# Kernel optimization log

Hardware: AMD Instinct MI355X
Metric: run time of the kernel (lower is better)

The kernel has to match this reference:

```python
import jax, jax.numpy as jnp
import numpy as np
from math import sqrt

B, S, E, D, O = 8, 2048, 1024, 128, 1024


def setup_inputs() -> dict:
    key = jax.random.key(0)
    ks = jax.random.split(key, 12)
    inp = {
        "query": jax.random.normal(ks[0], (B, S, E), jnp.float32),
        "key": jax.random.normal(ks[1], (B, S, E), jnp.float32),
        "value": jax.random.normal(ks[2], (B, S, E), jnp.float32),
        # causal (lower-triangular) mask, broadcastable over batch
        "mask": jnp.tril(jnp.ones((S, S), jnp.int32))[None, :, :],
        # linear params (torch Linear: y = x @ W.T + b); store as [in, out]
        "Wq": jax.random.normal(ks[3], (E, D), jnp.float32) / sqrt(E),
        "bq": jnp.zeros((D,), jnp.float32),
        "Wk": jax.random.normal(ks[4], (E, D), jnp.float32) / sqrt(E),
        "bk": jnp.zeros((D,), jnp.float32),
        "Wv": jax.random.normal(ks[5], (E, D), jnp.float32) / sqrt(E),
        "bv": jnp.zeros((D,), jnp.float32),
        "Wo": jax.random.normal(ks[6], (D, O), jnp.float32) / sqrt(D),
        "bo": jnp.zeros((O,), jnp.float32),
    }
    return inp


def reference(query, key, value, mask, Wq, bq, Wk, bk, Wv, bv, Wo, bo):
    q = jnp.einsum("bse,ed->bsd", query, Wq) + bq
    k = jnp.einsum("bse,ed->bsd", key, Wk) + bk
    v = jnp.einsum("bse,ed->bsd", value, Wv) + bv
    scale = 1.0 / sqrt(q.shape[-1])
    scores = jnp.einsum("bqd,bkd->bqk", q, k) * scale  # [B,S,S]
    scores = jnp.where(mask == 0, -jnp.inf, scores)
    weights = jax.nn.softmax(scores, axis=-1)
    weights = jnp.nan_to_num(weights)  # fully-masked rows -> 0, matching torch
    out = jnp.einsum("bqk,bkd->bqd", weights, v)
    return jnp.einsum("bqd,do->bqo", out, Wo) + bo
```

## Files before the change

kernel.cpp:

```cpp
#include <hip/hip_runtime.h>
#include <hip/hip_bf16.h>
#include <math.h>

#define B_ 8
#define S_ 2048
#define E_ 1024
#define D_ 128
#define O_ 1024
#define M_ (B_*S_)

typedef __bf16 bf16x8 __attribute__((ext_vector_type(8)));
typedef __bf16 bf16x4 __attribute__((ext_vector_type(4)));
typedef float  f32x4  __attribute__((ext_vector_type(4)));

#define MFMA16(a,b,c) __builtin_amdgcn_mfma_f32_16x16x32_bf16((a),(b),(c),0,0,0)

__global__ __launch_bounds__(256) void k_prep_weights(
    const float* __restrict__ Wq, const float* __restrict__ Wk,
    const float* __restrict__ Wv, const float* __restrict__ Wo,
    __bf16* __restrict__ Wtq, __bf16* __restrict__ Wtk,
    __bf16* __restrict__ Wtv, __bf16* __restrict__ Wot)
{
    const int bid = blockIdx.x;
    const int job = bid >> 7;
    const int within = bid & 127;

    const float* in;
    __bf16* outp;
    int R, C, bx, by;
    if (job < 3) {
        R = E_; C = D_;
        bx = within & 3; by = within >> 2;
        in   = (job == 0) ? Wq  : (job == 1) ? Wk  : Wv;
        outp = (job == 0) ? Wtq : (job == 1) ? Wtk : Wtv;
    } else {
        R = D_; C = O_;
        bx = within & 31; by = within >> 5;
        in = Wo; outp = Wot;
    }

    __shared__ float tile[32][33];
    const int tx = threadIdx.x, ty = threadIdx.y;
    int x = bx * 32 + tx;
    #pragma unroll
    for (int i = 0; i < 4; ++i) {
        int y = by * 32 + ty + i * 8;
        tile[ty + i * 8][tx] = in[(size_t)y * C + x];
    }
    __syncthreads();
    int xo = by * 32 + tx;
    #pragma unroll
    for (int i = 0; i < 4; ++i) {
        int yo = bx * 32 + ty + i * 8;
        outp[(size_t)yo * R + xo] = (__bf16)tile[tx][ty + i * 8];
    }
}

__global__ __launch_bounds__(256) void k_qkv_proj(
    const float* __restrict__ Xq, const float* __restrict__ Xk, const float* __restrict__ Xv,
    const __bf16* __restrict__ Wtq, const __bf16* __restrict__ Wtk, const __bf16* __restrict__ Wtv,
    const float* __restrict__ bq, const float* __restrict__ bk, const float* __restrict__ bv,
    __bf16* __restrict__ Qb, __bf16* __restrict__ Kb, __bf16* __restrict__ Vt)
{
    const int z = blockIdx.y;
    const float*  X    = (z == 0) ? Xq  : (z == 1) ? Xk  : Xv;
    const __bf16* Wt   = (z == 0) ? Wtq : (z == 1) ? Wtk : Wtv;
    const float*  bias = (z == 0) ? bq  : (z == 1) ? bk  : bv;

    __shared__ __align__(16) __bf16 As[128][40];
    __shared__ __align__(16) __bf16 Bs[128][40];

    const int tid  = threadIdx.x;
    const int lane = tid & 63;
    const int w    = tid >> 6;
    const int wr   = w >> 1, wc = w & 1;
    const int g    = lane >> 4, lr = lane & 15;
    const int m0   = blockIdx.x * 128;

    f32x4 acc[4][4] = {};

    for (int k0 = 0; k0 < E_; k0 += 32) {
        #pragma unroll
        for (int i = 0; i < 4; ++i) {
            int f = tid + i * 256;
            int row = f >> 3, c4 = f & 7;
            float4 v = *reinterpret_cast<const float4*>(X + (size_t)(m0 + row) * E_ + k0 + c4 * 4);
            bf16x4 h = { (__bf16)v.x, (__bf16)v.y, (__bf16)v.z, (__bf16)v.w };
            *reinterpret_cast<bf16x4*>(&As[row][c4 * 4]) = h;
        }
        #pragma unroll
        for (int i = 0; i < 2; ++i) {
            int f = tid + i * 256;
            int row = f >> 2, c8 = f & 3;
            bf16x8 v = *reinterpret_cast<const bf16x8*>(Wt + (size_t)row * E_ + k0 + c8 * 8);
            *reinterpret_cast<bf16x8*>(&Bs[row][c8 * 8]) = v;
        }
        __syncthreads();
        bf16x8 af[4], bfr[4];
        #pragma unroll
        for (int mi = 0; mi < 4; ++mi)
            af[mi] = *reinterpret_cast<const bf16x8*>(&As[wr * 64 + mi * 16 + lr][g * 8]);
        #pragma unroll
        for (int ni = 0; ni < 4; ++ni)
            bfr[ni] = *reinterpret_cast<const bf16x8*>(&Bs[wc * 64 + ni * 16 + lr][g * 8]);
        #pragma unroll
        for (int mi = 0; mi < 4; ++mi)
            #pragma unroll
            for (int ni = 0; ni < 4; ++ni)
                acc[mi][ni] = MFMA16(af[mi], bfr[ni], acc[mi][ni]);
        __syncthreads();
    }

    #pragma unroll
    for (int mi = 0; mi < 4; ++mi) {
        #pragma unroll
        for (int ni = 0; ni < 4; ++ni) {
            #pragma unroll
            for (int r = 0; r < 4; ++r) {
                int row = m0 + wr * 64 + mi * 16 + 4 * g + r;
                int col = wc * 64 + ni * 16 + lr;
                float v = acc[mi][ni][r] + bias[col];
                if (z == 0)      Qb[(size_t)row * D_ + col] = (__bf16)v;
                else if (z == 1) Kb[(size_t)row * D_ + col] = (__bf16)v;
                else {
                    int b = row >> 11, s = row & (S_ - 1);
                    Vt[((size_t)b * D_ + col) * S_ + s] = (__bf16)v;
                }
            }
        }
    }
}

__global__ __launch_bounds__(256) void k_attn(
    const __bf16* __restrict__ Q, const __bf16* __restrict__ K,
    const __bf16* __restrict__ Vt, __bf16* __restrict__ Ab)
{
    __shared__ __align__(16) __bf16 Ks[2][64][136];
    __shared__ __align__(16) __bf16 Vs[2][128][72];
    __shared__ __align__(16) __bf16 P[4][16][72];

    const int tid  = threadIdx.x;
    const int lane = tid & 63;
    const int w    = tid >> 6;
    const int g    = lane >> 4, lr = lane & 15;

    const int b     = blockIdx.x & 7;
    const int tq    = blockIdx.x >> 3;
    const int qbase = tq * 64;
    const int nch   = tq + 1;

    const __bf16* Qp  = Q  + (size_t)b * S_ * D_;
    const __bf16* Kp  = K  + (size_t)b * S_ * D_;
    const __bf16* Vtp = Vt + (size_t)b * D_ * S_;

    const float NEG_INF = -__builtin_inff();
    const float scale   = 0.08838834764831845f;

    const int krow = tid >> 2, kcb = (tid & 3) * 32;
    const int vrow = tid >> 1, vcb = (tid & 1) * 32;

    bf16x8 qf[4];
    #pragma unroll
    for (int dc = 0; dc < 4; ++dc)
        qf[dc] = *reinterpret_cast<const bf16x8*>(
            Qp + (size_t)(qbase + w * 16 + lr) * D_ + dc * 32 + g * 8);

    f32x4 o[8] = {};
    float m[4], l[4];
    #pragma unroll
    for (int r = 0; r < 4; ++r) { m[r] = NEG_INF; l[r] = 0.f; }

    bf16x8 kreg[4], vreg[4];

    {
        const __bf16* ks = Kp + (size_t)krow * D_ + kcb;
        const __bf16* vs = Vtp + (size_t)vrow * S_ + vcb;
        #pragma unroll
        for (int i = 0; i < 4; ++i) kreg[i] = *reinterpret_cast<const bf16x8*>(ks + i * 8);
        #pragma unroll
        for (int i = 0; i < 4; ++i) vreg[i] = *reinterpret_cast<const bf16x8*>(vs + i * 8);
        #pragma unroll
        for (int i = 0; i < 4; ++i) *reinterpret_cast<bf16x8*>(&Ks[0][krow][kcb + i * 8]) = kreg[i];
        #pragma unroll
        for (int i = 0; i < 4; ++i) *reinterpret_cast<bf16x8*>(&Vs[0][vrow][vcb + i * 8]) = vreg[i];
    }
    __syncthreads();

    for (int j = 0; j < nch; ++j) {
        const int  buf = j & 1;
        const bool pre = (j + 1 < nch);

        if (pre) {
            const int kv1 = (j + 1) * 64;
            const __bf16* ks = Kp + (size_t)(kv1 + krow) * D_ + kcb;
            const __bf16* vs = Vtp + (size_t)vrow * S_ + kv1 + vcb;
            #pragma unroll
            for (int i = 0; i < 4; ++i) kreg[i] = *reinterpret_cast<const bf16x8*>(ks + i * 8);
            #pragma unroll
            for (int i = 0; i < 4; ++i) vreg[i] = *reinterpret_cast<const bf16x8*>(vs + i * 8);
        }

        f32x4 s[4] = {};
        #pragma unroll
        for (int c = 0; c < 4; ++c) {
            #pragma unroll
            for (int dc = 0; dc < 4; ++dc) {
                bf16x8 kf = *reinterpret_cast<const bf16x8*>(&Ks[buf][c * 16 + lr][dc * 32 + g * 8]);
                s[c] = MFMA16(qf[dc], kf, s[c]);
            }
        }

        float p[4][4];
        float mt[4] = { NEG_INF, NEG_INF, NEG_INF, NEG_INF };
        if (j == tq) {
            #pragma unroll
            for (int c = 0; c < 4; ++c)
                #pragma unroll
                for (int r = 0; r < 4; ++r) {
                    float v = (c * 16 + lr <= w * 16 + 4 * g + r) ? s[c][r] * scale : NEG_INF;
                    p[c][r] = v;
                    mt[r] = fmaxf(mt[r], v);
                }
        } else {
            #pragma unroll
            for (int c = 0; c < 4; ++c)
                #pragma unroll
                for (int r = 0; r < 4; ++r) {
                    float v = s[c][r] * scale;
                    p[c][r] = v;
                    mt[r] = fmaxf(mt[r], v);
                }
        }
        #pragma unroll
        for (int off = 1; off < 16; off <<= 1)
            #pragma unroll
            for (int r = 0; r < 4; ++r)
                mt[r] = fmaxf(mt[r], __shfl_xor(mt[r], off));

        float corr[4], ts[4] = {0.f, 0.f, 0.f, 0.f};
        #pragma unroll
        for (int r = 0; r < 4; ++r) {
            float mn = fmaxf(m[r], mt[r]);
            corr[r] = __expf(m[r] - mn);
            m[r] = mn;
        }
        #pragma unroll
        for (int c = 0; c < 4; ++c)
            #pragma unroll
            for (int r = 0; r < 4; ++r) {
                float e = __expf(p[c][r] - m[r]);
                p[c][r] = e;
                ts[r] += e;
            }
        #pragma unroll
        for (int off = 1; off < 16; off <<= 1)
            #pragma unroll
            for (int r = 0; r < 4; ++r)
                ts[r] += __shfl_xor(ts[r], off);
        #pragma unroll
        for (int r = 0; r < 4; ++r) l[r] = l[r] * corr[r] + ts[r];
        #pragma unroll
        for (int dt = 0; dt < 8; ++dt)
            #pragma unroll
            for (int r = 0; r < 4; ++r)
                o[dt][r] *= corr[r];

        #pragma unroll
        for (int c = 0; c < 4; ++c)
            #pragma unroll
            for (int r = 0; r < 4; ++r)
                P[w][4 * g + r][c * 16 + lr] = (__bf16)p[c][r];
        bf16x8 pf[2];
        #pragma unroll
        for (int kc = 0; kc < 2; ++kc)
            pf[kc] = *reinterpret_cast<const bf16x8*>(&P[w][lr][kc * 32 + g * 8]);

        #pragma unroll
        for (int dt = 0; dt < 8; ++dt) {
            #pragma unroll
            for (int kc = 0; kc < 2; ++kc) {
                bf16x8 vf = *reinterpret_cast<const bf16x8*>(&Vs[buf][dt * 16 + lr][kc * 32 + g * 8]);
                o[dt] = MFMA16(pf[kc], vf, o[dt]);
            }
        }

        if (pre) {
            const int nb = buf ^ 1;
            #pragma unroll
            for (int i = 0; i < 4; ++i) *reinterpret_cast<bf16x8*>(&Ks[nb][krow][kcb + i * 8]) = kreg[i];
            #pragma unroll
            for (int i = 0; i < 4; ++i) *reinterpret_cast<bf16x8*>(&Vs[nb][vrow][vcb + i * 8]) = vreg[i];
            __syncthreads();
        }
    }

    float inv[4];
    #pragma unroll
    for (int r = 0; r < 4; ++r) inv[r] = 1.f / l[r];
    #pragma unroll
    for (int dt = 0; dt < 8; ++dt)
        #pragma unroll
        for (int r = 0; r < 4; ++r)
            Ab[((size_t)b * S_ + qbase + w * 16 + 4 * g + r) * D_ + dt * 16 + lr] =
                (__bf16)(o[dt][r] * inv[r]);
}

__global__ __launch_bounds__(256) void k_out_proj(
    const __bf16* __restrict__ A, const __bf16* __restrict__ Wot,
    const float* __restrict__ bo, float* __restrict__ out)
{
    __shared__ __align__(16) __bf16 As[128][40];
    __shared__ __align__(16) __bf16 Bs[128][40];

    const int tid  = threadIdx.x;
    const int lane = tid & 63;
    const int w    = tid >> 6;
    const int wr   = w >> 1, wc = w & 1;
    const int g    = lane >> 4, lr = lane & 15;
    const int m0   = blockIdx.x * 128;
    const int n0   = blockIdx.y * 128;

    f32x4 acc[4][4] = {};

    #pragma unroll
    for (int k0 = 0; k0 < D_; k0 += 32) {
        #pragma unroll
        for (int i = 0; i < 2; ++i) {
            int f = tid + i * 256;
            int row = f >> 2, c8 = f & 3;
            *reinterpret_cast<bf16x8*>(&As[row][c8 * 8]) =
                *reinterpret_cast<const bf16x8*>(A + (size_t)(m0 + row) * D_ + k0 + c8 * 8);
            *reinterpret_cast<bf16x8*>(&Bs[row][c8 * 8]) =
                *reinterpret_cast<const bf16x8*>(Wot + (size_t)(n0 + row) * D_ + k0 + c8 * 8);
        }
        __syncthreads();
        bf16x8 af[4], bfr[4];
        #pragma unroll
        for (int mi = 0; mi < 4; ++mi)
            af[mi] = *reinterpret_cast<const bf16x8*>(&As[wr * 64 + mi * 16 + lr][g * 8]);
        #pragma unroll
        for (int ni = 0; ni < 4; ++ni)
            bfr[ni] = *reinterpret_cast<const bf16x8*>(&Bs[wc * 64 + ni * 16 + lr][g * 8]);
        #pragma unroll
        for (int mi = 0; mi < 4; ++mi)
            #pragma unroll
            for (int ni = 0; ni < 4; ++ni)
                acc[mi][ni] = MFMA16(af[mi], bfr[ni], acc[mi][ni]);
        __syncthreads();
    }

    #pragma unroll
    for (int mi = 0; mi < 4; ++mi)
        #pragma unroll
        for (int ni = 0; ni < 4; ++ni)
            #pragma unroll
            for (int r = 0; r < 4; ++r) {
                int row = m0 + wr * 64 + mi * 16 + 4 * g + r;
                int col = n0 + wc * 64 + ni * 16 + lr;
                out[(size_t)row * O_ + col] = acc[mi][ni][r] + bo[col];
            }
}

extern "C" void kernel_launch(void* const* d_in, const int* in_sizes, int n_in,
                              void* d_out, int out_size, void* d_ws, size_t ws_size,
                              hipStream_t stream)
{
    const float* query = (const float*)d_in[0];
    const float* key   = (const float*)d_in[1];
    const float* value = (const float*)d_in[2];
    const float* Wq = (const float*)d_in[4];
    const float* bq = (const float*)d_in[5];
    const float* Wk = (const float*)d_in[6];
    const float* bk = (const float*)d_in[7];
    const float* Wv = (const float*)d_in[8];
    const float* bv = (const float*)d_in[9];
    const float* Wo = (const float*)d_in[10];
    const float* bo = (const float*)d_in[11];
    float* out = (float*)d_out;

    __bf16* Qb  = (__bf16*)d_ws;
    __bf16* Kb  = Qb  + (size_t)M_ * D_;
    __bf16* Vt  = Kb  + (size_t)M_ * D_;
    __bf16* Ab  = Vt  + (size_t)M_ * D_;
    __bf16* Wtq = Ab  + (size_t)M_ * D_;
    __bf16* Wtk = Wtq + (size_t)E_ * D_;
    __bf16* Wtv = Wtk + (size_t)E_ * D_;
    __bf16* Wot = Wtv + (size_t)E_ * D_;

    k_prep_weights<<<512, dim3(32, 8), 0, stream>>>(Wq, Wk, Wv, Wo, Wtq, Wtk, Wtv, Wot);

    k_qkv_proj<<<dim3(M_ / 128, 3), 256, 0, stream>>>(
        query, key, value, Wtq, Wtk, Wtv, bq, bk, bv, Qb, Kb, Vt);

    k_attn<<<256, 256, 0, stream>>>(Qb, Kb, Vt, Ab);

    k_out_proj<<<dim3(M_ / 128, O_ / 128), 256, 0, stream>>>(Ab, Wot, bo, out);
}
```

Measured before the change: 335.8 us.

## Double-buffer QKV projection with register prefetch and halve M tile

The QKV projection kernel now prefetches the next K-slice of activations and weights into registers while MFMAs run on the current shared-memory buffer, then writes into a second LDS buffer with one barrier per iteration. The M tile shrinks from 128 to 64 rows, doubling the grid to raise occupancy and wave count across CUs. The aim is to hide global-load latency on this memory-bound fp32-input GEMM, at the cost of more weight re-reads per block and extra register use.

```diff
diff --git a/kernel.cpp b/kernel.cpp
--- a/kernel.cpp
+++ b/kernel.cpp
@@ -67,57 +67,83 @@
     const __bf16* Wt   = (z == 0) ? Wtq : (z == 1) ? Wtk : Wtv;
     const float*  bias = (z == 0) ? bq  : (z == 1) ? bk  : bv;
 
-    __shared__ __align__(16) __bf16 As[128][40];
-    __shared__ __align__(16) __bf16 Bs[128][40];
+    __shared__ __align__(16) __bf16 As[2][64][40];
+    __shared__ __align__(16) __bf16 Bs[2][128][40];
 
     const int tid  = threadIdx.x;
     const int lane = tid & 63;
     const int w    = tid >> 6;
     const int wr   = w >> 1, wc = w & 1;
     const int g    = lane >> 4, lr = lane & 15;
-    const int m0   = blockIdx.x * 128;
-
-    f32x4 acc[4][4] = {};
-
-    for (int k0 = 0; k0 < E_; k0 += 32) {
-        #pragma unroll
-        for (int i = 0; i < 4; ++i) {
-            int f = tid + i * 256;
-            int row = f >> 3, c4 = f & 7;
-            float4 v = *reinterpret_cast<const float4*>(X + (size_t)(m0 + row) * E_ + k0 + c4 * 4);
-            bf16x4 h = { (__bf16)v.x, (__bf16)v.y, (__bf16)v.z, (__bf16)v.w };
-            *reinterpret_cast<bf16x4*>(&As[row][c4 * 4]) = h;
-        }
-        #pragma unroll
-        for (int i = 0; i < 2; ++i) {
-            int f = tid + i * 256;
-            int row = f >> 2, c8 = f & 3;
-            bf16x8 v = *reinterpret_cast<const bf16x8*>(Wt + (size_t)row * E_ + k0 + c8 * 8);
-            *reinterpret_cast<bf16x8*>(&Bs[row][c8 * 8]) = v;
-        }
-        __syncthreads();
-        bf16x8 af[4], bfr[4];
-        #pragma unroll
-        for (int mi = 0; mi < 4; ++mi)
-            af[mi] = *reinterpret_cast<const bf16x8*>(&As[wr * 64 + mi * 16 + lr][g * 8]);
+    const int m0   = blockIdx.x * 64;
+
+    const int ar0 = tid >> 3,          ac0 = (tid & 7) * 4;
+    const int ar1 = (tid + 256) >> 3,  ac1 = ac0;
+    const int br0 = tid >> 2,          bc0 = (tid & 3) * 8;
+    const int br1 = (tid + 256) >> 2,  bc1 = bc0;
+
+    f32x4 acc[2][4] = {};
+    float4 areg0, areg1;
+    bf16x8 breg0, breg1;
+
+    areg0 = *reinterpret_cast<const float4*>(X + (size_t)(m0 + ar0) * E_ + ac0);
+    areg1 = *reinterpret_cast<const float4*>(X + (size_t)(m0 + ar1) * E_ + ac1);
+    breg0 = *reinterpret_cast<const bf16x8*>(Wt + (size_t)br0 * E_ + bc0);
+    breg1 = *reinterpret_cast<const bf16x8*>(Wt + (size_t)br1 * E_ + bc1);
+    {
+        bf16x4 h0 = { (__bf16)areg0.x, (__bf16)areg0.y, (__bf16)areg0.z, (__bf16)areg0.w };
+        bf16x4 h1 = { (__bf16)areg1.x, (__bf16)areg1.y, (__bf16)areg1.z, (__bf16)areg1.w };
+        *reinterpret_cast<bf16x4*>(&As[0][ar0][ac0]) = h0;
+        *reinterpret_cast<bf16x4*>(&As[0][ar1][ac1]) = h1;
+        *reinterpret_cast<bf16x8*>(&Bs[0][br0][bc0]) = breg0;
+        *reinterpret_cast<bf16x8*>(&Bs[0][br1][bc1]) = breg1;
+    }
+    __syncthreads();
+
+    for (int j = 0; j < E_ / 32; ++j) {
+        const int  buf = j & 1;
+        const bool pre = (j + 1 < E_ / 32);
+
+        if (pre) {
+            const int k1 = (j + 1) * 32;
+            areg0 = *reinterpret_cast<const float4*>(X + (size_t)(m0 + ar0) * E_ + k1 + ac0);
+            areg1 = *reinterpret_cast<const float4*>(X + (size_t)(m0 + ar1) * E_ + k1 + ac1);
+            breg0 = *reinterpret_cast<const bf16x8*>(Wt + (size_t)br0 * E_ + k1 + bc0);
+            breg1 = *reinterpret_cast<const bf16x8*>(Wt + (size_t)br1 * E_ + k1 + bc1);
+        }
+
+        bf16x8 af[2], bfr[4];
+        #pragma unroll
+        for (int mi = 0; mi < 2; ++mi)
+            af[mi] = *reinterpret_cast<const bf16x8*>(&As[buf][wr * 32 + mi * 16 + lr][g * 8]);
         #pragma unroll
         for (int ni = 0; ni < 4; ++ni)
-            bfr[ni] = *reinterpret_cast<const bf16x8*>(&Bs[wc * 64 + ni * 16 + lr][g * 8]);
-        #pragma unroll
-        for (int mi = 0; mi < 4; ++mi)
+            bfr[ni] = *reinterpret_cast<const bf16x8*>(&Bs[buf][wc * 64 + ni * 16 + lr][g * 8]);
+        #pragma unroll
+        for (int mi = 0; mi < 2; ++mi)
             #pragma unroll
             for (int ni = 0; ni < 4; ++ni)
                 acc[mi][ni] = MFMA16(af[mi], bfr[ni], acc[mi][ni]);
-        __syncthreads();
-    }
-
-    #pragma unroll
-    for (int mi = 0; mi < 4; ++mi) {
+
+        if (pre) {
+            const int nb = buf ^ 1;
+            bf16x4 h0 = { (__bf16)areg0.x, (__bf16)areg0.y, (__bf16)areg0.z, (__bf16)areg0.w };
+            bf16x4 h1 = { (__bf16)areg1.x, (__bf16)areg1.y, (__bf16)areg1.z, (__bf16)areg1.w };
+            *reinterpret_cast<bf16x4*>(&As[nb][ar0][ac0]) = h0;
+            *reinterpret_cast<bf16x4*>(&As[nb][ar1][ac1]) = h1;
+            *reinterpret_cast<bf16x8*>(&Bs[nb][br0][bc0]) = breg0;
+            *reinterpret_cast<bf16x8*>(&Bs[nb][br1][bc1]) = breg1;
+            __syncthreads();
+        }
+    }
+
+    #pragma unroll
+    for (int mi = 0; mi < 2; ++mi) {
         #pragma unroll
         for (int ni = 0; ni < 4; ++ni) {
             #pragma unroll
             for (int r = 0; r < 4; ++r) {
-                int row = m0 + wr * 64 + mi * 16 + 4 * g + r;
+                int row = m0 + wr * 32 + mi * 16 + 4 * g + r;
                 int col = wc * 64 + ni * 16 + lr;
                 float v = acc[mi][ni][r] + bias[col];
                 if (z == 0)      Qb[(size_t)row * D_ + col] = (__bf16)v;
@@ -389,7 +415,7 @@
 
     k_prep_weights<<<512, dim3(32, 8), 0, stream>>>(Wq, Wk, Wv, Wo, Wtq, Wtk, Wtv, Wot);
 
-    k_qkv_proj<<<dim3(M_ / 128, 3), 256, 0, stream>>>(
+    k_qkv_proj<<<dim3(M_ / 64, 3), 256, 0, stream>>>(
         query, key, value, Wtq, Wtk, Wtv, bq, bk, bv, Qb, Kb, Vt);
 
     k_attn<<<256, 256, 0, stream>>>(Qb, Kb, Vt, Ab);
```

Measured after the change: 344.9 us. +2.7%, slower.
